# Kernel optimization log

Measured on AMD Instinct MI355X. Metric: run time of the kernel, lower is better.

Reference implementation:

```python
import jax, jax.numpy as jnp
import numpy as np

B, T, D, E, H = 4, 2048, 1024, 8, 4096

def setup_inputs() -> dict:
    key = jax.random.key(0)
    ks = jax.random.split(key, 10)
    s = 0.02
    return {
        "x": jax.random.normal(ks[0], (B, T, D), dtype=jnp.float32),
        "gate_w": jax.random.normal(ks[1], (D, E), dtype=jnp.float32) * s,
        "gate_b": jnp.zeros((E,), dtype=jnp.float32),
        "w1": jax.random.normal(ks[2], (E, D, H), dtype=jnp.float32) * s,
        "b1": jnp.zeros((E, H), dtype=jnp.float32),
        "w2": jax.random.normal(ks[3], (E, D, H), dtype=jnp.float32) * s,
        "b2": jnp.zeros((E, H), dtype=jnp.float32),
        "wp": jax.random.normal(ks[4], (E, H, D), dtype=jnp.float32) * s,
        "bp": jnp.zeros((E, D), dtype=jnp.float32),
        "k": 2,
    }

def reference(x, gate_w, gate_b, w1, b1, w2, b2, wp, bp, k):
    Bq, Tq, Dq = x.shape
    Eq = gate_w.shape[1]
    xf = x.reshape(-1, Dq)                          # [N, D]
    logits = xf @ gate_w + gate_b                   # [N, E]
    topk_scores, topk_idx = jax.lax.top_k(logits, k)  # [N, k]
    gate_probs = jax.nn.softmax(topk_scores, axis=-1)  # [N, k]
    onehot = jax.nn.one_hot(topk_idx, Eq, dtype=x.dtype)  # [N, k, E]
    # per-token per-expert combine weight (0 if expert not in top-k)
    combine = jnp.einsum('nk,nke->ne', gate_probs, onehot)  # [N, E]
    expert_counts = onehot.sum(axis=(0, 1))               # [E]
    out = jnp.zeros_like(xf)
    for e in range(Eq):  # small static loop over experts
        h = jax.nn.silu(xf @ w1[e] + b1[e]) * (xf @ w2[e] + b2[e])  # [N, H]
        y = h @ wp[e] + bp[e]                                       # [N, D]
        out = out + combine[:, e:e + 1] * y
    aux = jnp.sum((expert_counts / expert_counts.sum() - 1.0 / Eq) ** 2)
    return out.reshape(Bq, Tq, Dq), aux
```

## Files before the change

kernel.cpp:

```cpp
#include <hip/hip_runtime.h>
#include <cstdint>
#include <cstddef>

#define N_TOK 8192
#define DIM   1024
#define NEXP  8
#define HID   4096
#define WELEM 4194304ull

typedef __attribute__((ext_vector_type(8))) short short8v;
typedef __attribute__((ext_vector_type(8))) unsigned short ushort8v;
typedef __attribute__((ext_vector_type(4))) unsigned short ushort4v;
typedef __attribute__((ext_vector_type(4))) float f32x4;

__device__ __forceinline__ unsigned short f2bf(float f) {
  unsigned u = __builtin_bit_cast(unsigned, f);
  u += 0x7fffu + ((u >> 16) & 1u);
  return (unsigned short)(u >> 16);
}

__device__ __forceinline__ void gload16(const void* g, void* l) {
  __builtin_amdgcn_global_load_lds(
      (const __attribute__((address_space(1))) void*)g,
      (__attribute__((address_space(3))) void*)l, 16, 0, 0);
}

__global__ void gate2_k(const float* __restrict__ x, const float* __restrict__ gw,
                        const float* __restrict__ gb, int* __restrict__ tassign,
                        float2* __restrict__ tprob, unsigned short* __restrict__ xb) {
  int lane = threadIdx.x & 63, wid = threadIdx.x >> 6;
  int t = blockIdx.x * 4 + wid;
  const float* xr = x + (size_t)t * DIM;
  unsigned short* xbr = xb + (size_t)t * DIM;
  float acc[NEXP];
#pragma unroll
  for (int e = 0; e < NEXP; ++e) acc[e] = 0.f;
#pragma unroll
  for (int j = 0; j < DIM / 256; ++j) {
    int d0 = j * 256 + lane * 4;
    float4 xv = *(const float4*)(xr + d0);
    ushort4v o;
    o[0] = f2bf(xv.x); o[1] = f2bf(xv.y); o[2] = f2bf(xv.z); o[3] = f2bf(xv.w);
    *(ushort4v*)(xbr + d0) = o;
    const float* gp = gw + (size_t)d0 * NEXP;
#pragma unroll
    for (int c = 0; c < 4; ++c) {
      float xs = (c == 0) ? xv.x : (c == 1) ? xv.y : (c == 2) ? xv.z : xv.w;
      float4 g0 = *(const float4*)(gp + c * NEXP);
      float4 g1 = *(const float4*)(gp + c * NEXP + 4);
      acc[0] += xs * g0.x; acc[1] += xs * g0.y; acc[2] += xs * g0.z; acc[3] += xs * g0.w;
      acc[4] += xs * g1.x; acc[5] += xs * g1.y; acc[6] += xs * g1.z; acc[7] += xs * g1.w;
    }
  }
#pragma unroll
  for (int e = 0; e < NEXP; ++e) {
    float v = acc[e];
#pragma unroll
    for (int s = 1; s < 64; s <<= 1) v += __shfl_xor(v, s);
    acc[e] = v;
  }
  if (lane == 0) {
    float lg[NEXP];
#pragma unroll
    for (int e = 0; e < NEXP; ++e) lg[e] = acc[e] + gb[e];
    int i0 = 0;
#pragma unroll
    for (int e = 1; e < NEXP; ++e) if (lg[e] > lg[i0]) i0 = e;
    int i1 = -1;
#pragma unroll
    for (int e = 0; e < NEXP; ++e) if (e != i0 && (i1 < 0 || lg[e] > lg[i1])) i1 = e;
    float ex = expf(lg[i1] - lg[i0]);
    float p0 = 1.f / (1.f + ex);
    float p1 = ex * p0;
    tassign[t] = i0 | (i1 << 8);
    tprob[t] = make_float2(p0, p1);
  }
}

__global__ void route_k(const int* __restrict__ tassign, const float2* __restrict__ tprob,
                        int* __restrict__ rtok, float* __restrict__ rwgt,
                        int* __restrict__ counts, int* __restrict__ ebase) {
  __shared__ int h[NEXP];
  __shared__ int cur[NEXP];
  int tid = threadIdx.x;
  if (tid < NEXP) h[tid] = 0;
  __syncthreads();
  for (int t = tid; t < N_TOK; t += 256) {
    int a = tassign[t];
    atomicAdd(&h[a & 255], 1);
    atomicAdd(&h[(a >> 8) & 255], 1);
  }
  __syncthreads();
  if (tid == 0) {
    int b = 0;
    for (int e = 0; e < NEXP; ++e) { counts[e] = h[e]; ebase[e] = b; cur[e] = b; b += h[e]; }
  }
  __syncthreads();
  for (int t = tid; t < N_TOK; t += 256) {
    int a = tassign[t];
    float2 p = tprob[t];
    int p0 = atomicAdd(&cur[a & 255], 1);
    rtok[p0] = t; rwgt[p0] = p.x;
    int p1 = atomicAdd(&cur[(a >> 8) & 255], 1);
    rtok[p1] = t; rwgt[p1] = p.y;
  }
}

__global__ void aux_k(const int* __restrict__ counts, float* __restrict__ out) {
  if (threadIdx.x == 0) {
    float tot = 0.f, c[NEXP];
    for (int e = 0; e < NEXP; ++e) { c[e] = (float)counts[e]; tot += c[e]; }
    float a = 0.f;
    for (int e = 0; e < NEXP; ++e) { float d = c[e] / tot - 0.125f; a += d * d; }
    out[(size_t)N_TOK * DIM] = a;
  }
}

__global__ void tcvt_k(const float* __restrict__ w1, const float* __restrict__ w2,
                       const float* __restrict__ wp, unsigned short* __restrict__ d1,
                       unsigned short* __restrict__ d2, unsigned short* __restrict__ d3) {
  int tile = blockIdx.x, mat = blockIdx.y;
  size_t eo = (size_t)blockIdx.z * WELEM;
  const float* src; unsigned short* dst; int R, C;
  if (mat == 0)      { src = w1 + eo; dst = d1 + eo; R = DIM; C = HID; }
  else if (mat == 1) { src = w2 + eo; dst = d2 + eo; R = DIM; C = HID; }
  else               { src = wp + eo; dst = d3 + eo; R = HID; C = DIM; }
  int tilesC = C >> 6;
  int tr = (tile / tilesC) << 6;
  int tc = (tile % tilesC) << 6;
  __shared__ float tl[64][65];
  int tid = threadIdx.x;
  int lr = tid >> 4;
  int lc = (tid & 15) << 2;
#pragma unroll
  for (int i = 0; i < 4; ++i) {
    float4 v = *(const float4*)(src + (size_t)(tr + lr + i * 16) * C + tc + lc);
    tl[lr + i * 16][lc]     = v.x;
    tl[lr + i * 16][lc + 1] = v.y;
    tl[lr + i * 16][lc + 2] = v.z;
    tl[lr + i * 16][lc + 3] = v.w;
  }
  __syncthreads();
  int oc = tid >> 3;
  int orr = (tid & 7) << 3;
#pragma unroll
  for (int i = 0; i < 2; ++i) {
    int c = oc + i * 32;
    ushort8v v;
#pragma unroll
    for (int k = 0; k < 8; ++k) v[k] = f2bf(tl[orr + k][c]);
    *(ushort8v*)(dst + (size_t)(tc + c) * R + tr + orr) = v;
  }
}

template<int DUMMY>
__global__ __launch_bounds__(256, 4) void gemm12m_k(
    const unsigned short* __restrict__ xb,
    const unsigned short* __restrict__ w1b, const unsigned short* __restrict__ w2b,
    const float* __restrict__ b1, const float* __restrict__ b2,
    const int* __restrict__ rtok, const int* __restrict__ counts,
    const int* __restrict__ ebase, const int* __restrict__ gbase,
    unsigned short* __restrict__ Gx, int e0) {
  int f = blockIdx.x + gridDim.x * (blockIdx.y + gridDim.y * blockIdx.z);
  int total = gridDim.x * gridDim.y * gridDim.z;
  int cpx = total >> 3;
  int nf = (f & 7) * cpx + (f >> 3);
  int pe = gridDim.x * gridDim.y;
  int ez = nf / pe;
  int r  = nf - ez * pe;
  int ntb = r >> 5;
  int mt  = r & 31;

  const int e = e0 + ez;
  const int ce = counts[e];
  if (mt * 128 >= ce) return;
  const int rb = ebase[e];
  const int gb_ = gbase[e];
  const unsigned short* w1t = w1b + (size_t)ez * WELEM;
  const unsigned short* w2t = w2b + (size_t)ez * WELEM;
  const float* b1e = b1 + (size_t)e * HID;
  const float* b2e = b2 + (size_t)e * HID;

  __shared__ __attribute__((aligned(16))) unsigned short sA[128 * 64];
  __shared__ __attribute__((aligned(16))) unsigned short sB1[64 * 64];
  __shared__ __attribute__((aligned(16))) unsigned short sB2[64 * 64];

  const int tid = threadIdx.x;
  const int lane = tid & 63, wid = tid >> 6;
  const int wm = wid >> 1, wn = wid & 1;
  const unsigned stg = (unsigned)(wid * 1024);

  const int grow = tid >> 3;
  const int lcol = ((tid & 7) ^ (grow & 7)) << 3;
  int sl0 = mt * 128 + grow;
  int c0 = sl0 < ce ? sl0 : ce - 1;
  int c1 = sl0 + 32 < ce ? sl0 + 32 : ce - 1;
  int c2 = sl0 + 64 < ce ? sl0 + 64 : ce - 1;
  int c3 = sl0 + 96 < ce ? sl0 + 96 : ce - 1;
  const unsigned short* pa0 = xb + (size_t)rtok[rb + c0] * DIM + lcol;
  const unsigned short* pa1 = xb + (size_t)rtok[rb + c1] * DIM + lcol;
  const unsigned short* pa2 = xb + (size_t)rtok[rb + c2] * DIM + lcol;
  const unsigned short* pa3 = xb + (size_t)rtok[rb + c3] * DIM + lcol;
  const unsigned short* pq1 = w1t + (size_t)(ntb * 64 + grow) * DIM + lcol;
  const unsigned short* pq2 = w2t + (size_t)(ntb * 64 + grow) * DIM + lcol;

  f32x4 acc1[4][2] = {};
  f32x4 acc2[4][2] = {};

#pragma unroll 1
  for (int t = 0; t < 16; ++t) {
    const int k0 = t * 64;
    __syncthreads();
    gload16(pa0 + k0, (char*)sA + stg);
    gload16(pa1 + k0, (char*)sA + stg + 4096);
    gload16(pa2 + k0, (char*)sA + stg + 8192);
    gload16(pa3 + k0, (char*)sA + stg + 12288);
    gload16(pq1 + k0, (char*)sB1 + stg);
    gload16(pq1 + k0 + 32 * DIM, (char*)sB1 + stg + 4096);
    gload16(pq2 + k0, (char*)sB2 + stg);
    gload16(pq2 + k0 + 32 * DIM, (char*)sB2 + stg + 4096);
    __syncthreads();
#pragma unroll
    for (int s = 0; s < 2; ++s) {
      short8v af[4], bf1[2], bf2[2];
#pragma unroll
      for (int m = 0; m < 4; ++m) {
        int row = wm * 64 + m * 16 + (lane & 15);
        int p = (s * 4 + (lane >> 4)) ^ (row & 7);
        af[m] = *(const short8v*)((const char*)sA + row * 128 + p * 16);
      }
#pragma unroll
      for (int n = 0; n < 2; ++n) {
        int row = wn * 32 + n * 16 + (lane & 15);
        int p = (s * 4 + (lane >> 4)) ^ (row & 7);
        bf1[n] = *(const short8v*)((const char*)sB1 + row * 128 + p * 16);
        bf2[n] = *(const short8v*)((const char*)sB2 + row * 128 + p * 16);
      }
#pragma unroll
      for (int m = 0; m < 4; ++m)
#pragma unroll
        for (int n = 0; n < 2; ++n) {
          acc1[m][n] = __builtin_amdgcn_mfma_f32_16x16x32_bf16(af[m], bf1[n], acc1[m][n], 0, 0, 0);
          acc2[m][n] = __builtin_amdgcn_mfma_f32_16x16x32_bf16(af[m], bf2[n], acc2[m][n], 0, 0, 0);
        }
    }
  }

#pragma unroll
  for (int n = 0; n < 2; ++n) {
    int col = ntb * 64 + wn * 32 + n * 16 + (lane & 15);
    float bb1 = b1e[col], bb2 = b2e[col];
#pragma unroll
    for (int m = 0; m < 4; ++m) {
      int rbase = mt * 128 + wm * 64 + m * 16 + ((lane >> 4) << 2);
#pragma unroll
      for (int r2 = 0; r2 < 4; ++r2) {
        int slot = rbase + r2;
        if (slot < ce) {
          float h1 = acc1[m][n][r2] + bb1;
          float h2 = acc2[m][n][r2] + bb2;
          float sg = 1.0f / (1.0f + __expf(-h1));
          Gx[(size_t)(gb_ + slot) * HID + col] = f2bf(h1 * sg * h2);
        }
      }
    }
  }
}

#define STG(SD, P0, P1, P2, P3, K0)                                 \
  gload16(P0 + (K0), (char*)SD + stg);                              \
  gload16(P1 + (K0), (char*)SD + stg + 4096);                       \
  gload16(P2 + (K0), (char*)SD + stg + 8192);                       \
  gload16(P3 + (K0), (char*)SD + stg + 12288);

#define CMP()                                                       \
  {                                                                 \
    _Pragma("unroll")                                               \
    for (int s = 0; s < 2; ++s) {                                   \
      short8v af[4], bf[4];                                         \
      _Pragma("unroll")                                             \
      for (int m = 0; m < 4; ++m) {                                 \
        int row = wm * 64 + m * 16 + (lane & 15);                   \
        int p = (s * 4 + (lane >> 4)) ^ (row & 7);                  \
        af[m] = *(const short8v*)((const char*)sA + row * 128 + p * 16); \
      }                                                             \
      _Pragma("unroll")                                             \
      for (int n = 0; n < 4; ++n) {                                 \
        int row = wn * 64 + n * 16 + (lane & 15);                   \
        int p = (s * 4 + (lane >> 4)) ^ (row & 7);                  \
        bf[n] = *(const short8v*)((const char*)sB + row * 128 + p * 16); \
      }                                                             \
      _Pragma("unroll")                                             \
      for (int m = 0; m < 4; ++m)                                   \
        _Pragma("unroll")                                           \
        for (int n = 0; n < 4; ++n)                                 \
          acc[m][n] = __builtin_amdgcn_mfma_f32_16x16x32_bf16(af[m], bf[n], acc[m][n], 0, 0, 0); \
    }                                                               \
  }

#define GEMM_LOOP(NTILE)                                            \
  _Pragma("unroll 1")                                               \
  for (int t = 0; t < (NTILE); ++t) {                               \
    __syncthreads();                                                \
    STG(sA, pa0, pa1, pa2, pa3, t * 64);                            \
    STG(sB, pb0, pb1, pb2, pb3, t * 64);                            \
    __syncthreads();                                                \
    CMP();                                                          \
  }

__global__ __launch_bounds__(256, 4) void gemm3n_k(
    const unsigned short* __restrict__ Gx, const unsigned short* __restrict__ wpb,
    const float* __restrict__ bp, const int* __restrict__ rtok,
    const float* __restrict__ rwgt, const int* __restrict__ counts,
    const int* __restrict__ ebase, const int* __restrict__ gbase,
    float* __restrict__ out, int e0) {
  int f = blockIdx.x + gridDim.x * (blockIdx.y + gridDim.y * blockIdx.z);
  int total = gridDim.x * gridDim.y * gridDim.z;
  int cpx = total >> 3;
  int nf = (f & 7) * cpx + (f >> 3);
  int pe = gridDim.x * gridDim.y;
  int ez = nf / pe;
  int r  = nf - ez * pe;
  int ntb = r >> 5;
  int mt  = r & 31;

  const int e = e0 + ez;
  const int ce = counts[e];
  if (mt * 128 >= ce) return;
  const int rb = ebase[e];
  const int gb_ = gbase[e];
  const unsigned short* wpt = wpb + (size_t)ez * WELEM;
  const float* bpe = bp + (size_t)e * DIM;

  __shared__ __attribute__((aligned(16))) unsigned short sA[128 * 64];
  __shared__ __attribute__((aligned(16))) unsigned short sB[128 * 64];

  const int tid = threadIdx.x;
  const int lane = tid & 63, wid = tid >> 6;
  const int wm = wid >> 1, wn = wid & 1;
  const unsigned stg = (unsigned)(wid * 1024);

  const int grow = tid >> 3;
  const int lcol = ((tid & 7) ^ (grow & 7)) << 3;
  int sl0 = mt * 128 + grow;
  int c0 = sl0 < ce ? sl0 : ce - 1;
  int c1 = sl0 + 32 < ce ? sl0 + 32 : ce - 1;
  int c2 = sl0 + 64 < ce ? sl0 + 64 : ce - 1;
  int c3 = sl0 + 96 < ce ? sl0 + 96 : ce - 1;
  const unsigned short* pa0 = Gx + (size_t)(gb_ + c0) * HID + lcol;
  const unsigned short* pa1 = Gx + (size_t)(gb_ + c1) * HID + lcol;
  const unsigned short* pa2 = Gx + (size_t)(gb_ + c2) * HID + lcol;
  const unsigned short* pa3 = Gx + (size_t)(gb_ + c3) * HID + lcol;
  const unsigned short* pb0 = wpt + (size_t)(ntb * 128 + grow) * HID + lcol;
  const unsigned short* pb1 = pb0 + (size_t)32 * HID;
  const unsigned short* pb2 = pb0 + (size_t)64 * HID;
  const unsigned short* pb3 = pb0 + (size_t)96 * HID;

  f32x4 acc[4][4] = {};
  GEMM_LOOP(64);

#pragma unroll
  for (int n = 0; n < 4; ++n) {
    int col = ntb * 128 + wn * 64 + n * 16 + (lane & 15);
    float bb = bpe[col];
#pragma unroll
    for (int m = 0; m < 4; ++m) {
      int rbase = mt * 128 + wm * 64 + m * 16 + ((lane >> 4) << 2);
#pragma unroll
      for (int r2 = 0; r2 < 4; ++r2) {
        int slot = rbase + r2;
        if (slot < ce) {
          int tok = rtok[rb + slot];
          float w = rwgt[rb + slot];
          atomicAdd(out + (size_t)tok * DIM + col, w * (acc[m][n][r2] + bb));
        }
      }
    }
  }
}

extern "C" void kernel_launch(void* const* d_in, const int* in_sizes, int n_in,
                              void* d_out, int out_size, void* d_ws, size_t ws_size,
                              hipStream_t stream) {
  const float* x  = (const float*)d_in[0];
  const float* gw = (const float*)d_in[1];
  const float* gb = (const float*)d_in[2];
  const float* w1 = (const float*)d_in[3];
  const float* b1 = (const float*)d_in[4];
  const float* w2 = (const float*)d_in[5];
  const float* b2 = (const float*)d_in[6];
  const float* wp = (const float*)d_in[7];
  const float* bp = (const float*)d_in[8];
  float* out = (float*)d_out;

  char* ws = (char*)d_ws;
  const size_t BIG_NEED = 352551008ull;
  bool big = ws_size >= BIG_NEED;

  unsigned short* xb = (unsigned short*)ws;
  unsigned short *Gp, *w1a, *w2a, *wpa;
  int* tassign; float2* tprob; int* rtok; float* rwgt; int* meta;
  if (big) {
    Gp  = (unsigned short*)(ws + 16777216);
    w1a = (unsigned short*)(ws + 150994944);
    w2a = (unsigned short*)(ws + 218103808);
    wpa = (unsigned short*)(ws + 285212672);
    tassign = (int*)(ws + 352321536);
    tprob   = (float2*)(ws + 352354304);
    rtok    = (int*)(ws + 352419840);
    rwgt    = (float*)(ws + 352485376);
    meta    = (int*)(ws + 352550912);
  } else {
    Gp  = (unsigned short*)(ws + 16777216);
    w1a = (unsigned short*)(ws + 83886080);
    w2a = (unsigned short*)(ws + 92274688);
    wpa = (unsigned short*)(ws + 100663296);
    tassign = (int*)(ws + 109051904);
    tprob   = (float2*)(ws + 109084672);
    rtok    = (int*)(ws + 109150208);
    rwgt    = (float*)(ws + 109215744);
    meta    = (int*)(ws + 109281280);
  }
  int* counts = meta;
  int* ebase  = meta + 8;
  int* zbase  = meta + 16;

  hipMemsetAsync(meta, 0, 96, stream);
  hipMemsetAsync(out, 0, (size_t)(N_TOK * DIM + 1) * sizeof(float), stream);

  gate2_k<<<N_TOK / 4, 256, 0, stream>>>(x, gw, gb, tassign, tprob, xb);
  route_k<<<1, 256, 0, stream>>>(tassign, tprob, rtok, rwgt, counts, ebase);
  aux_k<<<1, 64, 0, stream>>>(counts, out);

  if (big) {
    tcvt_k<<<dim3(1024, 3, NEXP), 256, 0, stream>>>(w1, w2, wp, w1a, w2a, wpa);
    gemm12m_k<0><<<dim3(32, 64, NEXP), 256, 0, stream>>>(
        xb, w1a, w2a, b1, b2, rtok, counts, ebase, ebase, Gp, 0);
    gemm3n_k<<<dim3(32, 8, NEXP), 256, 0, stream>>>(
        Gp, wpa, bp, rtok, rwgt, counts, ebase, ebase, out, 0);
  } else {
    for (int e = 0; e < NEXP; ++e) {
      tcvt_k<<<dim3(1024, 3, 1), 256, 0, stream>>>(
          w1 + (size_t)e * WELEM, w2 + (size_t)e * WELEM, wp + (size_t)e * WELEM,
          w1a, w2a, wpa);
      gemm12m_k<0><<<dim3(32, 64, 1), 256, 0, stream>>>(
          xb, w1a, w2a, b1, b2, rtok, counts, ebase, zbase, Gp, e);
      gemm3n_k<<<dim3(32, 8, 1), 256, 0, stream>>>(
          Gp, wpa, bp, rtok, rwgt, counts, ebase, zbase, out, e);
    }
  }
}
```

Baseline: 805.6 us.

## Triple-buffer LDS with async prefetch and 512-thread 256-row tiles in expert GEMMs

Both expert GEMM kernels move from 256-thread blocks with 128-row M tiles to 512-thread blocks with 256-row tiles. The single-buffered sync-load-sync loop becomes a 3-stage LDS ring: loads for step t+2 are issued before computing step t, with explicit vmcnt waits and barriers, and MFMA sections run at raised wave priority. The aim is to hide global-to-LDS latency behind compute and halve the number of barriers per tile. The cost is much higher LDS use per block, which lowers occupancy, and more wasted rows when an expert's token count is not a multiple of 256.

Result: slower. 1.251 ms (+55.3%).

```diff
diff --git a/kernel.cpp b/kernel.cpp
--- a/kernel.cpp
+++ b/kernel.cpp
@@ -24,6 +24,14 @@
       (const __attribute__((address_space(1))) void*)g,
       (__attribute__((address_space(3))) void*)l, 16, 0, 0);
 }
+
+#define VMW6 do { asm volatile("s_waitcnt vmcnt(6)" ::: "memory"); \
+                  __builtin_amdgcn_sched_barrier(0); } while (0)
+#define VMW0 do { asm volatile("s_waitcnt vmcnt(0)" ::: "memory"); \
+                  __builtin_amdgcn_sched_barrier(0); } while (0)
+#define BARRL do { asm volatile("s_waitcnt lgkmcnt(0)" ::: "memory"); \
+                   __builtin_amdgcn_s_barrier(); \
+                   __builtin_amdgcn_sched_barrier(0); } while (0)
 
 __global__ void gate2_k(const float* __restrict__ x, const float* __restrict__ gw,
                         const float* __restrict__ gb, int* __restrict__ tassign,
@@ -154,7 +162,7 @@
 }
 
 template<int DUMMY>
-__global__ __launch_bounds__(256, 4) void gemm12m_k(
+__global__ __launch_bounds__(512, 2) void gemm12m_k(
     const unsigned short* __restrict__ xb,
     const unsigned short* __restrict__ w1b, const unsigned short* __restrict__ w2b,
     const float* __restrict__ b1, const float* __restrict__ b2,
@@ -168,12 +176,12 @@
   int pe = gridDim.x * gridDim.y;
   int ez = nf / pe;
   int r  = nf - ez * pe;
-  int ntb = r >> 5;
-  int mt  = r & 31;
+  int ntb = r >> 4;
+  int mt  = r & 15;
 
   const int e = e0 + ez;
   const int ce = counts[e];
-  if (mt * 128 >= ce) return;
+  if (mt * 256 >= ce) return;
   const int rb = ebase[e];
   const int gb_ = gbase[e];
   const unsigned short* w1t = w1b + (size_t)ez * WELEM;
@@ -181,9 +189,9 @@
   const float* b1e = b1 + (size_t)e * HID;
   const float* b2e = b2 + (size_t)e * HID;
 
-  __shared__ __attribute__((aligned(16))) unsigned short sA[128 * 64];
-  __shared__ __attribute__((aligned(16))) unsigned short sB1[64 * 64];
-  __shared__ __attribute__((aligned(16))) unsigned short sB2[64 * 64];
+  __shared__ __attribute__((aligned(16))) unsigned short sA[3][256 * 64];
+  __shared__ __attribute__((aligned(16))) unsigned short sB1[3][64 * 64];
+  __shared__ __attribute__((aligned(16))) unsigned short sB2[3][64 * 64];
 
   const int tid = threadIdx.x;
   const int lane = tid & 63, wid = tid >> 6;
@@ -192,11 +200,11 @@
 
   const int grow = tid >> 3;
   const int lcol = ((tid & 7) ^ (grow & 7)) << 3;
-  int sl0 = mt * 128 + grow;
+  int sl0 = mt * 256 + grow;
   int c0 = sl0 < ce ? sl0 : ce - 1;
-  int c1 = sl0 + 32 < ce ? sl0 + 32 : ce - 1;
-  int c2 = sl0 + 64 < ce ? sl0 + 64 : ce - 1;
-  int c3 = sl0 + 96 < ce ? sl0 + 96 : ce - 1;
+  int c1 = sl0 + 64 < ce ? sl0 + 64 : ce - 1;
+  int c2 = sl0 + 128 < ce ? sl0 + 128 : ce - 1;
+  int c3 = sl0 + 192 < ce ? sl0 + 192 : ce - 1;
   const unsigned short* pa0 = xb + (size_t)rtok[rb + c0] * DIM + lcol;
   const unsigned short* pa1 = xb + (size_t)rtok[rb + c1] * DIM + lcol;
   const unsigned short* pa2 = xb + (size_t)rtok[rb + c2] * DIM + lcol;
@@ -207,44 +215,69 @@
   f32x4 acc1[4][2] = {};
   f32x4 acc2[4][2] = {};
 
+#define STAGE12(BUF, K0)                                            \
+  {                                                                 \
+    char* bA = (char*)sA[BUF];                                      \
+    gload16(pa0 + (K0), bA + stg);                                  \
+    gload16(pa1 + (K0), bA + stg + 8192);                           \
+    gload16(pa2 + (K0), bA + stg + 16384);                          \
+    gload16(pa3 + (K0), bA + stg + 24576);                          \
+    gload16(pq1 + (K0), (char*)sB1[BUF] + stg);                     \
+    gload16(pq2 + (K0), (char*)sB2[BUF] + stg);                     \
+    __builtin_amdgcn_sched_barrier(0);                              \
+  }
+
+#define CMP12(BUF)                                                  \
+  {                                                                 \
+    const char* bA = (const char*)sA[BUF];                          \
+    const char* bB1 = (const char*)sB1[BUF];                        \
+    const char* bB2 = (const char*)sB2[BUF];                        \
+    _Pragma("unroll")                                               \
+    for (int s = 0; s < 2; ++s) {                                   \
+      short8v af[4], bf1[2], bf2[2];                                \
+      _Pragma("unroll")                                             \
+      for (int m = 0; m < 4; ++m) {                                 \
+        int row = wm * 64 + m * 16 + (lane & 15);                   \
+        int p = (s * 4 + (lane >> 4)) ^ (row & 7);                  \
+        af[m] = *(const short8v*)(bA + row * 128 + p * 16);         \
+      }                                                             \
+      _Pragma("unroll")                                             \
+      for (int n = 0; n < 2; ++n) {                                 \
+        int row = wn * 32 + n * 16 + (lane & 15);                   \
+        int p = (s * 4 + (lane >> 4)) ^ (row & 7);                  \
+        bf1[n] = *(const short8v*)(bB1 + row * 128 + p * 16);       \
+        bf2[n] = *(const short8v*)(bB2 + row * 128 + p * 16);       \
+      }                                                             \
+      __builtin_amdgcn_s_setprio(1);                                \
+      _Pragma("unroll")                                             \
+      for (int m = 0; m < 4; ++m)                                   \
+        _Pragma("unroll")                                           \
+        for (int n = 0; n < 2; ++n) {                               \
+          acc1[m][n] = __builtin_amdgcn_mfma_f32_16x16x32_bf16(af[m], bf1[n], acc1[m][n], 0, 0, 0); \
+          acc2[m][n] = __builtin_amdgcn_mfma_f32_16x16x32_bf16(af[m], bf2[n], acc2[m][n], 0, 0, 0); \
+        }                                                           \
+      __builtin_amdgcn_s_setprio(0);                                \
+    }                                                               \
+  }
+
+  STAGE12(0, 0);
+  STAGE12(1, 64);
+  VMW6; BARRL;
+  int cur = 0;
 #pragma unroll 1
-  for (int t = 0; t < 16; ++t) {
-    const int k0 = t * 64;
-    __syncthreads();
-    gload16(pa0 + k0, (char*)sA + stg);
-    gload16(pa1 + k0, (char*)sA + stg + 4096);
-    gload16(pa2 + k0, (char*)sA + stg + 8192);
-    gload16(pa3 + k0, (char*)sA + stg + 12288);
-    gload16(pq1 + k0, (char*)sB1 + stg);
-    gload16(pq1 + k0 + 32 * DIM, (char*)sB1 + stg + 4096);
-    gload16(pq2 + k0, (char*)sB2 + stg);
-    gload16(pq2 + k0 + 32 * DIM, (char*)sB2 + stg + 4096);
-    __syncthreads();
-#pragma unroll
-    for (int s = 0; s < 2; ++s) {
-      short8v af[4], bf1[2], bf2[2];
-#pragma unroll
-      for (int m = 0; m < 4; ++m) {
-        int row = wm * 64 + m * 16 + (lane & 15);
-        int p = (s * 4 + (lane >> 4)) ^ (row & 7);
-        af[m] = *(const short8v*)((const char*)sA + row * 128 + p * 16);
-      }
-#pragma unroll
-      for (int n = 0; n < 2; ++n) {
-        int row = wn * 32 + n * 16 + (lane & 15);
-        int p = (s * 4 + (lane >> 4)) ^ (row & 7);
-        bf1[n] = *(const short8v*)((const char*)sB1 + row * 128 + p * 16);
-        bf2[n] = *(const short8v*)((const char*)sB2 + row * 128 + p * 16);
-      }
-#pragma unroll
-      for (int m = 0; m < 4; ++m)
-#pragma unroll
-        for (int n = 0; n < 2; ++n) {
-          acc1[m][n] = __builtin_amdgcn_mfma_f32_16x16x32_bf16(af[m], bf1[n], acc1[m][n], 0, 0, 0);
-          acc2[m][n] = __builtin_amdgcn_mfma_f32_16x16x32_bf16(af[m], bf2[n], acc2[m][n], 0, 0, 0);
-        }
-    }
-  }
+  for (int t = 0; t < 14; ++t) {
+    int fly = cur + 2; if (fly >= 3) fly -= 3;
+    STAGE12(fly, (t + 2) * 64);
+    CMP12(cur);
+    VMW6; BARRL;
+    cur = (cur == 2) ? 0 : cur + 1;
+  }
+  CMP12(cur);
+  VMW0; BARRL;
+  cur = (cur == 2) ? 0 : cur + 1;
+  CMP12(cur);
+#undef STAGE12
+#undef CMP12
 
 #pragma unroll
   for (int n = 0; n < 2; ++n) {
@@ -252,7 +285,7 @@
     float bb1 = b1e[col], bb2 = b2e[col];
 #pragma unroll
     for (int m = 0; m < 4; ++m) {
-      int rbase = mt * 128 + wm * 64 + m * 16 + ((lane >> 4) << 2);
+      int rbase = mt * 256 + wm * 64 + m * 16 + ((lane >> 4) << 2);
 #pragma unroll
       for (int r2 = 0; r2 < 4; ++r2) {
         int slot = rbase + r2;
@@ -267,48 +300,7 @@
   }
 }
 
-#define STG(SD, P0, P1, P2, P3, K0)                                 \
-  gload16(P0 + (K0), (char*)SD + stg);                              \
-  gload16(P1 + (K0), (char*)SD + stg + 4096);                       \
-  gload16(P2 + (K0), (char*)SD + stg + 8192);                       \
-  gload16(P3 + (K0), (char*)SD + stg + 12288);
-
-#define CMP()                                                       \
-  {                                                                 \
-    _Pragma("unroll")                                               \
-    for (int s = 0; s < 2; ++s) {                                   \
-      short8v af[4], bf[4];                                         \
-      _Pragma("unroll")                                             \
-      for (int m = 0; m < 4; ++m) {                                 \
-        int row = wm * 64 + m * 16 + (lane & 15);                   \
-        int p = (s * 4 + (lane >> 4)) ^ (row & 7);                  \
-        af[m] = *(const short8v*)((const char*)sA + row * 128 + p * 16); \
-      }                                                             \
-      _Pragma("unroll")                                             \
-      for (int n = 0; n < 4; ++n) {                                 \
-        int row = wn * 64 + n * 16 + (lane & 15);                   \
-        int p = (s * 4 + (lane >> 4)) ^ (row & 7);                  \
-        bf[n] = *(const short8v*)((const char*)sB + row * 128 + p * 16); \
-      }                                                             \
-      _Pragma("unroll")                                             \
-      for (int m = 0; m < 4; ++m)                                   \
-        _Pragma("unroll")                                           \
-        for (int n = 0; n < 4; ++n)                                 \
-          acc[m][n] = __builtin_amdgcn_mfma_f32_16x16x32_bf16(af[m], bf[n], acc[m][n], 0, 0, 0); \
-    }                                                               \
-  }
-
-#define GEMM_LOOP(NTILE)                                            \
-  _Pragma("unroll 1")                                               \
-  for (int t = 0; t < (NTILE); ++t) {                               \
-    __syncthreads();                                                \
-    STG(sA, pa0, pa1, pa2, pa3, t * 64);                            \
-    STG(sB, pb0, pb1, pb2, pb3, t * 64);                            \
-    __syncthreads();                                                \
-    CMP();                                                          \
-  }
-
-__global__ __launch_bounds__(256, 4) void gemm3n_k(
+__global__ __launch_bounds__(512, 2) void gemm3n_k(
     const unsigned short* __restrict__ Gx, const unsigned short* __restrict__ wpb,
     const float* __restrict__ bp, const int* __restrict__ rtok,
     const float* __restrict__ rwgt, const int* __restrict__ counts,
@@ -321,19 +313,19 @@
   int pe = gridDim.x * gridDim.y;
   int ez = nf / pe;
   int r  = nf - ez * pe;
-  int ntb = r >> 5;
-  int mt  = r & 31;
+  int ntb = r >> 4;
+  int mt  = r & 15;
 
   const int e = e0 + ez;
   const int ce = counts[e];
-  if (mt * 128 >= ce) return;
+  if (mt * 256 >= ce) return;
   const int rb = ebase[e];
   const int gb_ = gbase[e];
   const unsigned short* wpt = wpb + (size_t)ez * WELEM;
   const float* bpe = bp + (size_t)e * DIM;
 
-  __shared__ __attribute__((aligned(16))) unsigned short sA[128 * 64];
-  __shared__ __attribute__((aligned(16))) unsigned short sB[128 * 64];
+  __shared__ __attribute__((aligned(16))) unsigned short sA[3][256 * 64];
+  __shared__ __attribute__((aligned(16))) unsigned short sB[3][128 * 64];
 
   const int tid = threadIdx.x;
   const int lane = tid & 63, wid = tid >> 6;
@@ -342,22 +334,80 @@
 
   const int grow = tid >> 3;
   const int lcol = ((tid & 7) ^ (grow & 7)) << 3;
-  int sl0 = mt * 128 + grow;
+  int sl0 = mt * 256 + grow;
   int c0 = sl0 < ce ? sl0 : ce - 1;
-  int c1 = sl0 + 32 < ce ? sl0 + 32 : ce - 1;
-  int c2 = sl0 + 64 < ce ? sl0 + 64 : ce - 1;
-  int c3 = sl0 + 96 < ce ? sl0 + 96 : ce - 1;
+  int c1 = sl0 + 64 < ce ? sl0 + 64 : ce - 1;
+  int c2 = sl0 + 128 < ce ? sl0 + 128 : ce - 1;
+  int c3 = sl0 + 192 < ce ? sl0 + 192 : ce - 1;
   const unsigned short* pa0 = Gx + (size_t)(gb_ + c0) * HID + lcol;
   const unsigned short* pa1 = Gx + (size_t)(gb_ + c1) * HID + lcol;
   const unsigned short* pa2 = Gx + (size_t)(gb_ + c2) * HID + lcol;
   const unsigned short* pa3 = Gx + (size_t)(gb_ + c3) * HID + lcol;
   const unsigned short* pb0 = wpt + (size_t)(ntb * 128 + grow) * HID + lcol;
-  const unsigned short* pb1 = pb0 + (size_t)32 * HID;
-  const unsigned short* pb2 = pb0 + (size_t)64 * HID;
-  const unsigned short* pb3 = pb0 + (size_t)96 * HID;
+  const unsigned short* pb1 = pb0 + (size_t)64 * HID;
 
   f32x4 acc[4][4] = {};
-  GEMM_LOOP(64);
+
+#define STG3(BUF, K0)                                               \
+  {                                                                 \
+    char* bA = (char*)sA[BUF];                                      \
+    gload16(pa0 + (K0), bA + stg);                                  \
+    gload16(pa1 + (K0), bA + stg + 8192);                           \
+    gload16(pa2 + (K0), bA + stg + 16384);                          \
+    gload16(pa3 + (K0), bA + stg + 24576);                          \
+    char* bB = (char*)sB[BUF];                                      \
+    gload16(pb0 + (K0), bB + stg);                                  \
+    gload16(pb1 + (K0), bB + stg + 8192);                           \
+    __builtin_amdgcn_sched_barrier(0);                              \
+  }
+
+#define CMP3(BUF)                                                   \
+  {                                                                 \
+    const char* bA = (const char*)sA[BUF];                          \
+    const char* bB = (const char*)sB[BUF];                          \
+    _Pragma("unroll")                                               \
+    for (int s = 0; s < 2; ++s) {                                   \
+      short8v af[4], bf[4];                                         \
+      _Pragma("unroll")                                             \
+      for (int m = 0; m < 4; ++m) {                                 \
+        int row = wm * 64 + m * 16 + (lane & 15);                   \
+        int p = (s * 4 + (lane >> 4)) ^ (row & 7);                  \
+        af[m] = *(const short8v*)(bA + row * 128 + p * 16);         \
+      }                                                             \
+      _Pragma("unroll")                                             \
+      for (int n = 0; n < 4; ++n) {                                 \
+        int row = wn * 64 + n * 16 + (lane & 15);                   \
+        int p = (s * 4 + (lane >> 4)) ^ (row & 7);                  \
+        bf[n] = *(const short8v*)(bB + row * 128 + p * 16);         \
+      }                                                             \
+      __builtin_amdgcn_s_setprio(1);                                \
+      _Pragma("unroll")                                             \
+      for (int m = 0; m < 4; ++m)                                   \
+        _Pragma("unroll")                                           \
+        for (int n = 0; n < 4; ++n)                                 \
+          acc[m][n] = __builtin_amdgcn_mfma_f32_16x16x32_bf16(af[m], bf[n], acc[m][n], 0, 0, 0); \
+      __builtin_amdgcn_s_setprio(0);                                \
+    }                                                               \
+  }
+
+  STG3(0, 0);
+  STG3(1, 64);
+  VMW6; BARRL;
+  int cur = 0;
+#pragma unroll 1
+  for (int t = 0; t < 62; ++t) {
+    int fly = cur + 2; if (fly >= 3) fly -= 3;
+    STG3(fly, (t + 2) * 64);
+    CMP3(cur);
+    VMW6; BARRL;
+    cur = (cur == 2) ? 0 : cur + 1;
+  }
+  CMP3(cur);
+  VMW0; BARRL;
+  cur = (cur == 2) ? 0 : cur + 1;
+  CMP3(cur);
+#undef STG3
+#undef CMP3
 
 #pragma unroll
   for (int n = 0; n < 4; ++n) {
@@ -365,7 +415,7 @@
     float bb = bpe[col];
 #pragma unroll
     for (int m = 0; m < 4; ++m) {
-      int rbase = mt * 128 + wm * 64 + m * 16 + ((lane >> 4) << 2);
+      int rbase = mt * 256 + wm * 64 + m * 16 + ((lane >> 4) << 2);
 #pragma unroll
       for (int r2 = 0; r2 < 4; ++r2) {
         int slot = rbase + r2;
@@ -434,18 +484,18 @@
 
   if (big) {
     tcvt_k<<<dim3(1024, 3, NEXP), 256, 0, stream>>>(w1, w2, wp, w1a, w2a, wpa);
-    gemm12m_k<0><<<dim3(32, 64, NEXP), 256, 0, stream>>>(
+    gemm12m_k<0><<<dim3(16, 64, NEXP), 512, 0, stream>>>(
         xb, w1a, w2a, b1, b2, rtok, counts, ebase, ebase, Gp, 0);
-    gemm3n_k<<<dim3(32, 8, NEXP), 256, 0, stream>>>(
+    gemm3n_k<<<dim3(16, 8, NEXP), 512, 0, stream>>>(
         Gp, wpa, bp, rtok, rwgt, counts, ebase, ebase, out, 0);
   } else {
     for (int e = 0; e < NEXP; ++e) {
       tcvt_k<<<dim3(1024, 3, 1), 256, 0, stream>>>(
           w1 + (size_t)e * WELEM, w2 + (size_t)e * WELEM, wp + (size_t)e * WELEM,
           w1a, w2a, wpa);
-      gemm12m_k<0><<<dim3(32, 64, 1), 256, 0, stream>>>(
+      gemm12m_k<0><<<dim3(16, 64, 1), 512, 0, stream>>>(
           xb, w1a, w2a, b1, b2, rtok, counts, ebase, zbase, Gp, e);
-      gemm3n_k<<<dim3(32, 8, 1), 256, 0, stream>>>(
+      gemm3n_k<<<dim3(16, 8, 1), 512, 0, stream>>>(
           Gp, wpa, bp, rtok, rwgt, counts, ebase, zbase, out, e);
     }
   }
```
